# Kernel optimization log

Hardware: AMD Instinct MI355X
Metric: run time of the kernel (lower is better)

## Reference

```python
import jax, jax.numpy as jnp
import numpy as np

N_NODES = 50000


def _gcn_conv(x, edge_index, W, b, n_nodes):
    # PyG GCNConv: add self loops, symmetric normalization, then
    # out[dst] = sum_{src->dst} norm * (x[src] @ W) + b
    src, dst = edge_index[0], edge_index[1]
    loop = jnp.arange(n_nodes, dtype=src.dtype)
    src = jnp.concatenate([src, loop])
    dst = jnp.concatenate([dst, loop])
    deg = jax.ops.segment_sum(jnp.ones_like(src, dtype=x.dtype), dst, num_segments=n_nodes)
    dinv = jnp.where(deg > 0, jax.lax.rsqrt(deg), 0.0)
    norm = dinv[src] * dinv[dst]                      # [E+N]
    h = x @ W                                         # [N, out] dense GEMM first (in >= out here)
    msg = h[src] * norm[:, None]                      # gather + scale
    out = jax.ops.segment_sum(msg, dst, num_segments=n_nodes)  # scatter-add
    return out + b


def setup_inputs() -> dict:
    key = jax.random.key(0)
    k = jax.random.split(key, 5)
    in_c, hid_c, out_c = 128, 128, 64
    n, e = N_NODES, 800000
    x = jax.random.normal(k[0], (n, in_c), dtype=jnp.float32)
    edge_index = jax.random.randint(k[1], (2, e), 0, n, dtype=jnp.int64)
    # Glorot-ish scaled weights
    W1 = jax.random.normal(k[2], (in_c, hid_c), dtype=jnp.float32) * (1.0 / np.sqrt(in_c))
    b1 = jnp.zeros((hid_c,), dtype=jnp.float32)
    W2 = jax.random.normal(k[3], (hid_c, out_c), dtype=jnp.float32) * (1.0 / np.sqrt(hid_c))
    b2 = jnp.zeros((out_c,), dtype=jnp.float32)
    return {"x": x, "edge_index": edge_index, "W1": W1, "b1": b1, "W2": W2, "b2": b2}


def reference(x, edge_index, W1, b1, W2, b2):
    # Net.encode: conv1 -> relu -> conv2
    h = _gcn_conv(x, edge_index, W1, b1, N_NODES)
    h = jax.nn.relu(h)
    z = _gcn_conv(h, edge_index, W2, b2, N_NODES)
    return z
```

## Files before the change

### kernel.cpp

```cpp
#include <hip/hip_runtime.h>
#include <math.h>

constexpr int C_IN  = 128;
constexpr int C_HID = 128;
constexpr int C_OUT = 64;

typedef short bf8   __attribute__((ext_vector_type(8)));
typedef float f32x4 __attribute__((ext_vector_type(4)));

__device__ __forceinline__ int wave_incl_scan(int v, int lane) {
    #pragma unroll
    for (int off = 1; off < 64; off <<= 1) {
        int u = __shfl_up(v, off, 64);
        if (lane >= off) v += u;
    }
    return v;
}
__device__ __forceinline__ short b16(float f) {
    unsigned int u = __float_as_uint(f);
    u += 0x7FFFu + ((u >> 16) & 1u);
    return (short)(u >> 16);
}
__device__ __forceinline__ unsigned int bpack(float a, float b) {
    unsigned int ua = __float_as_uint(a), ub = __float_as_uint(b);
    ua += 0x7FFFu + ((ua >> 16) & 1u);
    ub += 0x7FFFu + ((ub >> 16) & 1u);
    return (ua >> 16) | (ub & 0xFFFF0000u);
}
__device__ __forceinline__ void acc4(float* a, const uint2 v) {
    a[0] += __uint_as_float(v.x << 16);
    a[1] += __uint_as_float(v.x & 0xFFFF0000u);
    a[2] += __uint_as_float(v.y << 16);
    a[3] += __uint_as_float(v.y & 0xFFFF0000u);
}
__device__ __forceinline__ void acc8(float* a, const uint4 v) {
    a[0] += __uint_as_float(v.x << 16);
    a[1] += __uint_as_float(v.x & 0xFFFF0000u);
    a[2] += __uint_as_float(v.y << 16);
    a[3] += __uint_as_float(v.y & 0xFFFF0000u);
    a[4] += __uint_as_float(v.z << 16);
    a[5] += __uint_as_float(v.z & 0xFFFF0000u);
    a[6] += __uint_as_float(v.w << 16);
    a[7] += __uint_as_float(v.w & 0xFFFF0000u);
}

__global__ __launch_bounds__(256) void k_zero(int* __restrict__ p, int n4) {
    int i = blockIdx.x * 256 + threadIdx.x;
    if (i < n4) reinterpret_cast<int4*>(p)[i] = make_int4(0, 0, 0, 0);
}

__global__ __launch_bounds__(256) void k_count2(const int* __restrict__ dst, int e,
                                                int* __restrict__ cnt,
                                                int* __restrict__ slot) {
    int i = blockIdx.x * 256 + threadIdx.x;
    if (i < e) slot[i] = atomicAdd(&cnt[dst[i]], 1);
}

__global__ __launch_bounds__(256) void k_scanA(const int* __restrict__ cnt, int n,
                                               int* __restrict__ rowstart,
                                               int* __restrict__ blocksum,
                                               float* __restrict__ dinv) {
    __shared__ int swave[4];
    const int tid = threadIdx.x, lane = tid & 63, w = tid >> 6;
    const int idx = blockIdx.x * 1024 + tid * 4;
    int4 c = make_int4(0, 0, 0, 0);
    if (idx + 3 < n) {
        c = *reinterpret_cast<const int4*>(cnt + idx);
    } else {
        if (idx + 0 < n) c.x = cnt[idx + 0];
        if (idx + 1 < n) c.y = cnt[idx + 1];
        if (idx + 2 < n) c.z = cnt[idx + 2];
        if (idx + 3 < n) c.w = cnt[idx + 3];
    }
    if (idx + 0 < n) dinv[idx + 0] = rsqrtf((float)(c.x + 1));
    if (idx + 1 < n) dinv[idx + 1] = rsqrtf((float)(c.y + 1));
    if (idx + 2 < n) dinv[idx + 2] = rsqrtf((float)(c.z + 1));
    if (idx + 3 < n) dinv[idx + 3] = rsqrtf((float)(c.w + 1));

    const int s4 = c.x + c.y + c.z + c.w;
    const int incl = wave_incl_scan(s4, lane);
    if (lane == 63) swave[w] = incl;
    __syncthreads();
    int base = incl - s4;
    #pragma unroll
    for (int j = 0; j < 4; ++j) if (j < w) base += swave[j];

    int4 o;
    o.x = base;
    o.y = base + c.x;
    o.z = base + c.x + c.y;
    o.w = base + c.x + c.y + c.z;
    *reinterpret_cast<int4*>(rowstart + idx) = o;

    if (tid == 0) blocksum[blockIdx.x] = swave[0] + swave[1] + swave[2] + swave[3];
}

__global__ __launch_bounds__(64) void k_scanB(const int* __restrict__ blocksum, int nb,
                                              int* __restrict__ blockoff,
                                              int* __restrict__ rowstart, int n) {
    const int lane = threadIdx.x;
    int v = (lane < nb) ? blocksum[lane] : 0;
    int incl = wave_incl_scan(v, lane);
    if (lane < nb) blockoff[lane] = incl - v;
    if (lane == 63) rowstart[n] = incl;
}

__global__ __launch_bounds__(256) void k_scanC(int* __restrict__ rowstart,
                                               const int* __restrict__ blockoff, int n) {
    const int idx = (blockIdx.x * 256 + threadIdx.x) * 4;
    if (idx >= n) return;
    const int off = blockoff[idx >> 10];
    if (idx + 3 < n) {
        int4 v = *reinterpret_cast<int4*>(rowstart + idx);
        v.x += off; v.y += off; v.z += off; v.w += off;
        *reinterpret_cast<int4*>(rowstart + idx) = v;
    } else {
        for (int i = idx; i < n; ++i) rowstart[i] += off;
    }
}

__global__ __launch_bounds__(256) void k_fill2(const int* __restrict__ src,
                                               const int* __restrict__ dst,
                                               const int* __restrict__ slot, int e,
                                               const int* __restrict__ rowstart,
                                               int* __restrict__ nbr) {
    int i = blockIdx.x * 256 + threadIdx.x;
    if (i >= e) return;
    nbr[rowstart[dst[i]] + slot[i]] = src[i];
}

__global__ __launch_bounds__(256) void k_gemm1m(const float* __restrict__ x,
                                                const float* __restrict__ W,
                                                const float* __restrict__ dinv,
                                                unsigned short* __restrict__ h1b,
                                                int n) {
    __shared__ short wf[8 * 4 * 64 * 8];
    const int tid = threadIdx.x;

    for (int i = tid; i < 2048; i += 256) {
        const int l = i & 63, kt = (i >> 6) & 3, ct = i >> 8;
        const int krow = kt * 32 + ((l >> 4) << 3);
        const int col  = ct * 16 + (l & 15);
        const float* wp = W + (size_t)krow * C_HID + col;
        uint4 u;
        u.x = bpack(wp[0 * C_HID], wp[1 * C_HID]);
        u.y = bpack(wp[2 * C_HID], wp[3 * C_HID]);
        u.z = bpack(wp[4 * C_HID], wp[5 * C_HID]);
        u.w = bpack(wp[6 * C_HID], wp[7 * C_HID]);
        reinterpret_cast<uint4*>(wf)[i] = u;
    }
    __syncthreads();

    const int l = tid & 63, w = tid >> 6;
    const int row0 = blockIdx.x * 64 + w * 16;
    int arow = row0 + (l & 15);
    if (arow >= n) arow = n - 1;
    const float* xr = x + (size_t)arow * C_IN + ((l >> 4) << 3);

    bf8 a[4];
    #pragma unroll
    for (int kt = 0; kt < 4; ++kt) {
        float4 p0 = *reinterpret_cast<const float4*>(xr + kt * 32);
        float4 p1 = *reinterpret_cast<const float4*>(xr + kt * 32 + 4);
        bf8 t;
        t[0] = b16(p0.x); t[1] = b16(p0.y); t[2] = b16(p0.z); t[3] = b16(p0.w);
        t[4] = b16(p1.x); t[5] = b16(p1.y); t[6] = b16(p1.z); t[7] = b16(p1.w);
        a[kt] = t;
    }

    f32x4 acc[8];
    #pragma unroll
    for (int ct = 0; ct < 8; ++ct) acc[ct] = (f32x4){0.f, 0.f, 0.f, 0.f};
    const bf8* bw = reinterpret_cast<const bf8*>(wf);
    #pragma unroll
    for (int kt = 0; kt < 4; ++kt)
        #pragma unroll
        for (int ct = 0; ct < 8; ++ct)
            acc[ct] = __builtin_amdgcn_mfma_f32_16x16x32_bf16(
                a[kt], bw[(ct * 4 + kt) * 64 + l], acc[ct], 0, 0, 0);

    const int rbase = row0 + ((l >> 4) << 2);
    float dv[4];
    #pragma unroll
    for (int r = 0; r < 4; ++r) {
        int rr = rbase + r;
        dv[r] = (rr < n) ? dinv[rr] : 0.f;
    }
    #pragma unroll
    for (int ct = 0; ct < 8; ++ct) {
        const int col = ct * 16 + (l & 15);
        #pragma unroll
        for (int r = 0; r < 4; ++r) {
            int rr = rbase + r;
            if (rr < n)
                h1b[(size_t)rr * C_HID + col] = (unsigned short)b16(acc[ct][r] * dv[r]);
        }
    }
}

__global__ __launch_bounds__(256) void k_agg1b(const unsigned int* __restrict__ h1b,
                                               const int* __restrict__ rowstart,
                                               const int* __restrict__ nbr,
                                               const float* __restrict__ dinv,
                                               const float* __restrict__ b1,
                                               unsigned int* __restrict__ actb,
                                               int n) {
    int node = blockIdx.x * 8 + (threadIdx.x >> 5);
    if (node >= n) return;
    const int c4 = threadIdx.x & 31;
    const uint2* h1v = reinterpret_cast<const uint2*>(h1b);
    float a[4] = {0.f, 0.f, 0.f, 0.f};
    acc4(a, h1v[node * 32 + c4]);
    int j   = rowstart[node];
    int end = rowstart[node + 1];
    for (; j + 1 < end; j += 2) {
        int s0 = nbr[j], s1 = nbr[j + 1];
        uint2 v0 = h1v[s0 * 32 + c4];
        uint2 v1 = h1v[s1 * 32 + c4];
        acc4(a, v0); acc4(a, v1);
    }
    if (j < end) acc4(a, h1v[nbr[j] * 32 + c4]);
    const float sc = dinv[node];
    const float4 bb = reinterpret_cast<const float4*>(b1)[c4];
    uint2 p;
    p.x = bpack(fmaxf(sc * a[0] + bb.x, 0.f), fmaxf(sc * a[1] + bb.y, 0.f));
    p.y = bpack(fmaxf(sc * a[2] + bb.z, 0.f), fmaxf(sc * a[3] + bb.w, 0.f));
    reinterpret_cast<uint2*>(actb)[node * 32 + c4] = p;
}

__global__ __launch_bounds__(256) void k_gemm2m(const unsigned short* __restrict__ actb,
                                                const float* __restrict__ W2,
                                                const float* __restrict__ dinv,
                                                unsigned short* __restrict__ h2b,
                                                int n) {
    __shared__ short wf[4 * 4 * 64 * 8];
    const int tid = threadIdx.x;

    for (int i = tid; i < 1024; i += 256) {
        const int l = i & 63, kt = (i >> 6) & 3, ct = i >> 8;
        const int krow = kt * 32 + ((l >> 4) << 3);
        const int col  = ct * 16 + (l & 15);
        const float* wp = W2 + (size_t)krow * C_OUT + col;
        uint4 u;
        u.x = bpack(wp[0 * C_OUT], wp[1 * C_OUT]);
        u.y = bpack(wp[2 * C_OUT], wp[3 * C_OUT]);
        u.z = bpack(wp[4 * C_OUT], wp[5 * C_OUT]);
        u.w = bpack(wp[6 * C_OUT], wp[7 * C_OUT]);
        reinterpret_cast<uint4*>(wf)[i] = u;
    }
    __syncthreads();

    const int l = tid & 63, w = tid >> 6;
    const int row0 = blockIdx.x * 64 + w * 16;
    int arow = row0 + (l & 15);
    if (arow >= n) arow = n - 1;
    const unsigned short* ar = actb + (size_t)arow * C_HID + ((l >> 4) << 3);

    bf8 a[4];
    #pragma unroll
    for (int kt = 0; kt < 4; ++kt)
        a[kt] = *reinterpret_cast<const bf8*>(ar + kt * 32);

    f32x4 acc[4];
    #pragma unroll
    for (int ct = 0; ct < 4; ++ct) acc[ct] = (f32x4){0.f, 0.f, 0.f, 0.f};
    const bf8* bw = reinterpret_cast<const bf8*>(wf);
    #pragma unroll
    for (int kt = 0; kt < 4; ++kt)
        #pragma unroll
        for (int ct = 0; ct < 4; ++ct)
            acc[ct] = __builtin_amdgcn_mfma_f32_16x16x32_bf16(
                a[kt], bw[(ct * 4 + kt) * 64 + l], acc[ct], 0, 0, 0);

    const int rbase = row0 + ((l >> 4) << 2);
    float dv[4];
    #pragma unroll
    for (int r = 0; r < 4; ++r) {
        int rr = rbase + r;
        dv[r] = (rr < n) ? dinv[rr] : 0.f;
    }
    #pragma unroll
    for (int ct = 0; ct < 4; ++ct) {
        const int col = ct * 16 + (l & 15);
        #pragma unroll
        for (int r = 0; r < 4; ++r) {
            int rr = rbase + r;
            if (rr < n)
                h2b[(size_t)rr * C_OUT + col] = (unsigned short)b16(acc[ct][r] * dv[r]);
        }
    }
}

__global__ __launch_bounds__(256) void k_agg2b(const unsigned int* __restrict__ h2b,
                                               const int* __restrict__ rowstart,
                                               const int* __restrict__ nbr,
                                               const float* __restrict__ dinv,
                                               const float* __restrict__ b2,
                                               float* __restrict__ outb, int n) {
    int node = blockIdx.x * 32 + (threadIdx.x >> 3);
    if (node >= n) return;
    const int lane8 = threadIdx.x & 7;
    const uint4* h2v = reinterpret_cast<const uint4*>(h2b);
    float a8[8] = {0.f, 0.f, 0.f, 0.f, 0.f, 0.f, 0.f, 0.f};
    acc8(a8, h2v[node * 8 + lane8]);
    int j   = rowstart[node];
    int end = rowstart[node + 1];
    for (; j + 1 < end; j += 2) {
        int s0 = nbr[j], s1 = nbr[j + 1];
        uint4 v0 = h2v[s0 * 8 + lane8];
        uint4 v1 = h2v[s1 * 8 + lane8];
        acc8(a8, v0); acc8(a8, v1);
    }
    if (j < end) acc8(a8, h2v[nbr[j] * 8 + lane8]);
    const float s = dinv[node];
    const float4 c0 = reinterpret_cast<const float4*>(b2)[2 * lane8 + 0];
    const float4 c1 = reinterpret_cast<const float4*>(b2)[2 * lane8 + 1];
    float4 o0, o1;
    o0.x = s * a8[0] + c0.x; o0.y = s * a8[1] + c0.y;
    o0.z = s * a8[2] + c0.z; o0.w = s * a8[3] + c0.w;
    o1.x = s * a8[4] + c1.x; o1.y = s * a8[5] + c1.y;
    o1.z = s * a8[6] + c1.z; o1.w = s * a8[7] + c1.w;
    reinterpret_cast<float4*>(outb)[node * 16 + 2 * lane8 + 0] = o0;
    reinterpret_cast<float4*>(outb)[node * 16 + 2 * lane8 + 1] = o1;
}

extern "C" void kernel_launch(void* const* d_in, const int* in_sizes, int n_in,
                              void* d_out, int out_size, void* d_ws, size_t ws_size,
                              hipStream_t stream) {
    const float* x  = (const float*)d_in[0];
    const int*   ei = (const int*)d_in[1];
    const float* W1 = (const float*)d_in[2];
    const float* b1 = (const float*)d_in[3];
    const float* W2 = (const float*)d_in[4];
    const float* b2 = (const float*)d_in[5];

    const int n = in_sizes[0] / C_IN;
    const int e = in_sizes[1] / 2;
    const int* src = ei;
    const int* dst = ei + e;

    char* ws = (char*)d_ws;
    float* dinv     = (float*)(ws);
    int*   cnt      = (int*)  (ws + (1u << 18));
    int*   rowstart = (int*)  (ws + (2u << 18));
    int*   blocksum = (int*)  (ws + (1u << 20));
    int*   blockoff = (int*)  (ws + (1u << 20) + 4096);
    int*   nbr      = (int*)  (ws + (2u << 20));
    int*   slot     = (int*)  (ws + (6u << 20));
    unsigned short* h1b  = (unsigned short*)(ws + (10u << 20));
    unsigned short* actb = (unsigned short*)(ws + (23u << 20));
    unsigned short* h2b  = (unsigned short*)(ws + (36u << 20));
    float* outb     = (float*)d_out;

    const int NB = (n + 1023) / 1024;
    const int n4 = (n + 3) / 4;

    k_zero  <<<(n4 + 255) / 256, 256, 0, stream>>>(cnt, n4);
    k_count2<<<(e + 255) / 256, 256, 0, stream>>>(dst, e, cnt, slot);
    k_scanA <<<NB, 256, 0, stream>>>(cnt, n, rowstart, blocksum, dinv);
    k_scanB <<<1, 64, 0, stream>>>(blocksum, NB, blockoff, rowstart, n);
    k_scanC <<<NB, 256, 0, stream>>>(rowstart, blockoff, n);
    k_fill2 <<<(e + 255) / 256, 256, 0, stream>>>(src, dst, slot, e, rowstart, nbr);
    k_gemm1m<<<(n + 63) / 64, 256, 0, stream>>>(x, W1, dinv, h1b, n);
    k_agg1b <<<(n + 7) / 8,   256, 0, stream>>>((const unsigned int*)h1b, rowstart, nbr, dinv, b1,
                                                (unsigned int*)actb, n);
    k_gemm2m<<<(n + 63) / 64, 256, 0, stream>>>(actb, W2, dinv, h2b, n);
    k_agg2b <<<(n + 31) / 32, 256, 0, stream>>>((const unsigned int*)h2b, rowstart, nbr, dinv, b2,
                                                outb, n);
}
```

Before: 142.9 us.

## Replicate degree counters across eight copies and store neighbor indices as 16-bit

Each block now counts degrees into one of eight replicated counter arrays, picked by block index, to spread atomic contention on hot destination nodes. The scan kernel sums the replicas and rewrites them in place as per-replica exclusive offsets, which the fill kernel uses to place each edge. The neighbor list shrinks from 32-bit to 16-bit indices, which halves the index traffic read by both aggregation kernels. The cost is eight times more counter memory to zero and scan, and node ids must stay below 65536.

```diff
diff --git a/kernel.cpp b/kernel.cpp
--- a/kernel.cpp
+++ b/kernel.cpp
@@ -4,6 +4,7 @@
 constexpr int C_IN  = 128;
 constexpr int C_HID = 128;
 constexpr int C_OUT = 64;
+constexpr int NREP  = 8;
 
 typedef short bf8   __attribute__((ext_vector_type(8)));
 typedef float f32x4 __attribute__((ext_vector_type(4)));
@@ -49,28 +50,44 @@
     if (i < n4) reinterpret_cast<int4*>(p)[i] = make_int4(0, 0, 0, 0);
 }
 
-__global__ __launch_bounds__(256) void k_count2(const int* __restrict__ dst, int e,
-                                                int* __restrict__ cnt,
-                                                int* __restrict__ slot) {
+__global__ __launch_bounds__(256) void k_count2r(const int* __restrict__ dst, int e, int n,
+                                                 int* __restrict__ cntr,
+                                                 int* __restrict__ slot) {
     int i = blockIdx.x * 256 + threadIdx.x;
-    if (i < e) slot[i] = atomicAdd(&cnt[dst[i]], 1);
-}
-
-__global__ __launch_bounds__(256) void k_scanA(const int* __restrict__ cnt, int n,
-                                               int* __restrict__ rowstart,
-                                               int* __restrict__ blocksum,
-                                               float* __restrict__ dinv) {
+    if (i >= e) return;
+    int r = blockIdx.x & (NREP - 1);
+    slot[i] = atomicAdd(&cntr[r * n + dst[i]], 1);
+}
+
+__global__ __launch_bounds__(256) void k_scanA8(int* __restrict__ cntr, int n,
+                                                int* __restrict__ rowstart,
+                                                int* __restrict__ blocksum,
+                                                float* __restrict__ dinv) {
     __shared__ int swave[4];
     const int tid = threadIdx.x, lane = tid & 63, w = tid >> 6;
     const int idx = blockIdx.x * 1024 + tid * 4;
     int4 c = make_int4(0, 0, 0, 0);
     if (idx + 3 < n) {
-        c = *reinterpret_cast<const int4*>(cnt + idx);
-    } else {
-        if (idx + 0 < n) c.x = cnt[idx + 0];
-        if (idx + 1 < n) c.y = cnt[idx + 1];
-        if (idx + 2 < n) c.z = cnt[idx + 2];
-        if (idx + 3 < n) c.w = cnt[idx + 3];
+        #pragma unroll
+        for (int r = 0; r < NREP; ++r) {
+            int4* p = reinterpret_cast<int4*>(cntr + (size_t)r * n + idx);
+            int4 t = *p;
+            *p = c;
+            c.x += t.x; c.y += t.y; c.z += t.z; c.w += t.w;
+        }
+    } else if (idx < n) {
+        for (int m = idx; m < n; ++m) {
+            int acc = 0;
+            #pragma unroll
+            for (int r = 0; r < NREP; ++r) {
+                int t = cntr[(size_t)r * n + m];
+                cntr[(size_t)r * n + m] = acc;
+                acc += t;
+            }
+            int q = m - idx;
+            if (q == 0) c.x = acc; else if (q == 1) c.y = acc;
+            else if (q == 2) c.z = acc; else c.w = acc;
+        }
     }
     if (idx + 0 < n) dinv[idx + 0] = rsqrtf((float)(c.x + 1));
     if (idx + 1 < n) dinv[idx + 1] = rsqrtf((float)(c.y + 1));
@@ -90,7 +107,7 @@
     o.y = base + c.x;
     o.z = base + c.x + c.y;
     o.w = base + c.x + c.y + c.z;
-    *reinterpret_cast<int4*>(rowstart + idx) = o;
+    if (idx < n) *reinterpret_cast<int4*>(rowstart + idx) = o;
 
     if (tid == 0) blocksum[blockIdx.x] = swave[0] + swave[1] + swave[2] + swave[3];
 }
@@ -119,14 +136,18 @@
     }
 }
 
-__global__ __launch_bounds__(256) void k_fill2(const int* __restrict__ src,
-                                               const int* __restrict__ dst,
-                                               const int* __restrict__ slot, int e,
-                                               const int* __restrict__ rowstart,
-                                               int* __restrict__ nbr) {
+__global__ __launch_bounds__(256) void k_fill2r(const int* __restrict__ src,
+                                                const int* __restrict__ dst,
+                                                const int* __restrict__ slot, int e, int n,
+                                                const int* __restrict__ rowstart,
+                                                const int* __restrict__ repoff,
+                                                unsigned short* __restrict__ nbr) {
     int i = blockIdx.x * 256 + threadIdx.x;
     if (i >= e) return;
-    nbr[rowstart[dst[i]] + slot[i]] = src[i];
+    int r = blockIdx.x & (NREP - 1);
+    int d = dst[i];
+    int pos = rowstart[d] + repoff[r * n + d] + slot[i];
+    nbr[pos] = (unsigned short)src[i];
 }
 
 __global__ __launch_bounds__(256) void k_gemm1m(const float* __restrict__ x,
@@ -200,7 +221,7 @@
 
 __global__ __launch_bounds__(256) void k_agg1b(const unsigned int* __restrict__ h1b,
                                                const int* __restrict__ rowstart,
-                                               const int* __restrict__ nbr,
+                                               const unsigned short* __restrict__ nbr,
                                                const float* __restrict__ dinv,
                                                const float* __restrict__ b1,
                                                unsigned int* __restrict__ actb,
@@ -293,7 +314,7 @@
 
 __global__ __launch_bounds__(256) void k_agg2b(const unsigned int* __restrict__ h2b,
                                                const int* __restrict__ rowstart,
-                                               const int* __restrict__ nbr,
+                                               const unsigned short* __restrict__ nbr,
                                                const float* __restrict__ dinv,
                                                const float* __restrict__ b2,
                                                float* __restrict__ outb, int n) {
@@ -341,30 +362,30 @@
 
     char* ws = (char*)d_ws;
     float* dinv     = (float*)(ws);
-    int*   cnt      = (int*)  (ws + (1u << 18));
     int*   rowstart = (int*)  (ws + (2u << 18));
     int*   blocksum = (int*)  (ws + (1u << 20));
     int*   blockoff = (int*)  (ws + (1u << 20) + 4096);
-    int*   nbr      = (int*)  (ws + (2u << 20));
-    int*   slot     = (int*)  (ws + (6u << 20));
+    int*   cntr     = (int*)  (ws + (2u << 20));
+    int*   slot     = (int*)  (ws + (4u << 20));
+    unsigned short* nbr  = (unsigned short*)(ws + (8u << 20));
     unsigned short* h1b  = (unsigned short*)(ws + (10u << 20));
     unsigned short* actb = (unsigned short*)(ws + (23u << 20));
     unsigned short* h2b  = (unsigned short*)(ws + (36u << 20));
     float* outb     = (float*)d_out;
 
     const int NB = (n + 1023) / 1024;
-    const int n4 = (n + 3) / 4;
-
-    k_zero  <<<(n4 + 255) / 256, 256, 0, stream>>>(cnt, n4);
-    k_count2<<<(e + 255) / 256, 256, 0, stream>>>(dst, e, cnt, slot);
-    k_scanA <<<NB, 256, 0, stream>>>(cnt, n, rowstart, blocksum, dinv);
-    k_scanB <<<1, 64, 0, stream>>>(blocksum, NB, blockoff, rowstart, n);
-    k_scanC <<<NB, 256, 0, stream>>>(rowstart, blockoff, n);
-    k_fill2 <<<(e + 255) / 256, 256, 0, stream>>>(src, dst, slot, e, rowstart, nbr);
-    k_gemm1m<<<(n + 63) / 64, 256, 0, stream>>>(x, W1, dinv, h1b, n);
-    k_agg1b <<<(n + 7) / 8,   256, 0, stream>>>((const unsigned int*)h1b, rowstart, nbr, dinv, b1,
-                                                (unsigned int*)actb, n);
-    k_gemm2m<<<(n + 63) / 64, 256, 0, stream>>>(actb, W2, dinv, h2b, n);
-    k_agg2b <<<(n + 31) / 32, 256, 0, stream>>>((const unsigned int*)h2b, rowstart, nbr, dinv, b2,
-                                                outb, n);
-}
+    const int nz4 = (NREP * n + 3) / 4;
+
+    k_zero   <<<(nz4 + 255) / 256, 256, 0, stream>>>(cntr, nz4);
+    k_count2r<<<(e + 255) / 256, 256, 0, stream>>>(dst, e, n, cntr, slot);
+    k_scanA8 <<<NB, 256, 0, stream>>>(cntr, n, rowstart, blocksum, dinv);
+    k_scanB  <<<1, 64, 0, stream>>>(blocksum, NB, blockoff, rowstart, n);
+    k_scanC  <<<NB, 256, 0, stream>>>(rowstart, blockoff, n);
+    k_fill2r <<<(e + 255) / 256, 256, 0, stream>>>(src, dst, slot, e, n, rowstart, cntr, nbr);
+    k_gemm1m <<<(n + 63) / 64, 256, 0, stream>>>(x, W1, dinv, h1b, n);
+    k_agg1b  <<<(n + 7) / 8,   256, 0, stream>>>((const unsigned int*)h1b, rowstart, nbr, dinv, b1,
+                                                 (unsigned int*)actb, n);
+    k_gemm2m <<<(n + 63) / 64, 256, 0, stream>>>(actb, W2, dinv, h2b, n);
+    k_agg2b  <<<(n + 31) / 32, 256, 0, stream>>>((const unsigned int*)h2b, rowstart, nbr, dinv, b2,
+                                                 outb, n);
+}
```

After: 139.7 us. -2.3%, faster.
